# Performance work log

Measured on AMD Instinct MI355X. Metric: run time of the kernel, lower is better.

Reference implementation:

```python
import jax, jax.numpy as jnp
import numpy as np

B = 65536
D_EMB = 512      # embedding_dim
D_SPD = 1        # speed_dim
D_LAT = 128      # speed_latent_dim
H = 256          # hidden_size
K = 6            # num_branch
D_IN = D_EMB + D_LAT  # 640, branch/speed-head input dim


def _lin(key, din, dout):
    kw, kb = jax.random.split(key)
    W = jax.random.normal(kw, (din, dout), dtype=jnp.float32) * 0.02
    b = jax.random.normal(kb, (dout,), dtype=jnp.float32) * 0.02
    return W, b


def setup_inputs() -> dict:
    key = jax.random.key(0)
    ks = jax.random.split(key, 16)
    embedding = jax.random.normal(ks[0], (B, D_EMB), dtype=jnp.float32)
    speed = jax.random.uniform(ks[1], (B, D_SPD), dtype=jnp.float32)
    command = jax.random.randint(ks[2], (B,), 1, K + 1, dtype=jnp.int32)  # values 1..6
    # speed input MLP: speed_dim -> H -> D_LAT
    Wsi1, bsi1 = _lin(ks[3], D_SPD, H)
    Wsi2, bsi2 = _lin(ks[4], H, D_LAT)
    # speed prediction head: D_IN -> H -> H -> speed_dim
    Wso1, bso1 = _lin(ks[5], D_IN, H)
    Wso2, bso2 = _lin(ks[6], H, H)
    Wso3, bso3 = _lin(ks[7], H, D_SPD)
    # K branch heads, stacked on leading axis: D_IN -> H -> H -> 3, sigmoid
    def _stack(key, din, dout):
        kw, kb = jax.random.split(key)
        W = jax.random.normal(kw, (K, din, dout), dtype=jnp.float32) * 0.02
        b = jax.random.normal(kb, (K, dout), dtype=jnp.float32) * 0.02
        return W, b
    Wb1, bb1 = _stack(ks[8], D_IN, H)
    Wb2, bb2 = _stack(ks[9], H, H)
    Wb3, bb3 = _stack(ks[10], H, 3)
    return dict(embedding=embedding, speed=speed, command=command,
                Wsi1=Wsi1, bsi1=bsi1, Wsi2=Wsi2, bsi2=bsi2,
                Wso1=Wso1, bso1=bso1, Wso2=Wso2, bso2=bso2, Wso3=Wso3, bso3=bso3,
                Wb1=Wb1, bb1=bb1, Wb2=Wb2, bb2=bb2, Wb3=Wb3, bb3=bb3)


def reference(embedding, speed, command,
              Wsi1, bsi1, Wsi2, bsi2,
              Wso1, bso1, Wso2, bso2, Wso3, bso3,
              Wb1, bb1, Wb2, bb2, Wb3, bb3):
    # speed -> latent
    sp = jax.nn.relu(speed @ Wsi1 + bsi1) @ Wsi2 + bsi2          # [B, D_LAT]
    emb = jnp.concatenate([embedding, sp], axis=1)               # [B, D_IN]
    # compute ALL K branch heads (as the original does), then mask by command
    h = jax.nn.relu(jnp.einsum('bd,kdh->bkh', emb, Wb1) + bb1)   # [B, K, H]
    h = jax.nn.relu(jnp.einsum('bkh,khj->bkj', h, Wb2) + bb2)    # [B, K, H]
    ctrl_all = jax.nn.sigmoid(jnp.einsum('bkh,kho->bko', h, Wb3) + bb3)  # [B, K, 3]
    mask = (command[:, None] - 1 == jnp.arange(K)[None, :]).astype(ctrl_all.dtype)  # [B, K]
    control_pred = jnp.sum(ctrl_all * mask[:, :, None], axis=1)  # [B, 3]
    # speed prediction head
    hs = jax.nn.relu(emb @ Wso1 + bso1)
    hs = jax.nn.relu(hs @ Wso2 + bso2)
    speed_pred = hs @ Wso3 + bso3                                # [B, 1]
    return control_pred, speed_pred
```

## Files before the change

kernel.cpp:

```cpp
#include <hip/hip_runtime.h>
#include <hip/hip_bf16.h>


#define NB 65536
#define NBRB 1030

typedef __attribute__((ext_vector_type(8))) short short8;
typedef __attribute__((ext_vector_type(4))) float f32x4;
typedef unsigned short bhalf;
typedef unsigned int u32;

__device__ __forceinline__ bhalf f2b(float x) {
    __hip_bfloat16 h = __float2bfloat16(x);
    return *reinterpret_cast<bhalf*>(&h);
}
__device__ __forceinline__ void gll16(const void* g, void* l) {
    __builtin_amdgcn_global_load_lds(
        (const __attribute__((address_space(1))) u32*)g,
        (__attribute__((address_space(3))) u32*)l, 16, 0, 0);
}
__device__ __forceinline__ int sadr(int row, int cb) {
    return row * 64 + (cb ^ (((row >> 1) & 3) << 4));
}
__device__ __forceinline__ int yadr(int row, int cb) {
    return row * 512 + (cb ^ ((row & 7) << 4));
}
__device__ __forceinline__ void wvm6() { asm volatile("s_waitcnt vmcnt(6)" ::: "memory"); }
__device__ __forceinline__ void wvm0() { asm volatile("s_waitcnt vmcnt(0)" ::: "memory"); }
__device__ __forceinline__ void wlgkm0() { asm volatile("s_waitcnt lgkmcnt(0)" ::: "memory"); }

__global__ __launch_bounds__(256) void k_wprep(
    const float* __restrict__ Wsi2, const float* __restrict__ Wso1,
    const float* __restrict__ Wso2, const float* __restrict__ Wb1,
    const float* __restrict__ Wb2,
    bhalf* __restrict__ Wsi2T, bhalf* __restrict__ Wso1T,
    bhalf* __restrict__ Wso2T, bhalf* __restrict__ Wb1T,
    bhalf* __restrict__ Wb2T) {
    __shared__ float T[64][65];
    const int id = blockIdx.x, t = threadIdx.x;
    const float* src; bhalf* dst; int K, N, tk, tn, b;
    if (id < 8)        { src = Wsi2; dst = Wsi2T; K = 256; N = 128; b = 0; int tl = id;      tk = tl / 2; tn = tl % 2; }
    else if (id < 48)  { src = Wso1; dst = Wso1T; K = 640; N = 256; b = 0; int tl = id - 8;  tk = tl / 4; tn = tl % 4; }
    else if (id < 64)  { src = Wso2; dst = Wso2T; K = 256; N = 256; b = 0; int tl = id - 48; tk = tl / 4; tn = tl % 4; }
    else if (id < 304) { src = Wb1;  dst = Wb1T;  K = 640; N = 256; int li = id - 64;  b = li / 40; int tl = li % 40; tk = tl / 4; tn = tl % 4; }
    else               { src = Wb2;  dst = Wb2T;  K = 256; N = 256; int li = id - 304; b = li / 16; int tl = li % 16; tk = tl / 4; tn = tl % 4; }
    const int k0 = tk * 64, n0 = tn * 64;
    src += (size_t)b * K * N; dst += (size_t)b * N * K;
    const int c = t & 63, r0 = t >> 6;
#pragma unroll
    for (int j = 0; j < 16; ++j) {
        int r = r0 + j * 4;
        T[r][c] = src[(size_t)(k0 + r) * N + n0 + c];
    }
    __syncthreads();
#pragma unroll
    for (int j = 0; j < 16; ++j) {
        int r = r0 + j * 4;
        dst[(size_t)(n0 + r) * K + k0 + c] = f2b(T[c][r]);
    }
}

__global__ __launch_bounds__(256) void k_prep(
    const float* __restrict__ speed, const float* __restrict__ Wsi1,
    const float* __restrict__ bsi1, const bhalf* __restrict__ Wsi2T,
    const float* __restrict__ bsi2, const int* __restrict__ cmd,
    bhalf* __restrict__ spb, int* __restrict__ bcnt) {
    __shared__ bhalf A[64 * 72];
    __shared__ bhalf BT[128 * 72];
    const int t = threadIdx.x, lane = t & 63, wid = t >> 6;
    const int rbase = blockIdx.x * 64;
    if (wid == 0) {
        int c = cmd[rbase + lane] - 1;
        int v = 0;
#pragma unroll
        for (int g = 0; g < 6; ++g) {
            unsigned long long m = __ballot(c == g);
            if (lane == g) v = (int)__popcll(m);
        }
        if (lane < 6) bcnt[blockIdx.x * 6 + lane] = v;
    }
    const int wm = wid >> 1, wn = wid & 1;
    f32x4 acc[2][4];
    for (int m = 0; m < 2; ++m) for (int n = 0; n < 4; ++n)
        for (int r = 0; r < 4; ++r) acc[m][n][r] = 0.f;
    const int ar = t >> 2, kp = (t & 3) * 16;
    const float s = speed[rbase + ar];
    for (int kc = 0; kc < 4; ++kc) {
        short8 w0, w1;
#pragma unroll
        for (int j = 0; j < 8; ++j) {
            int k = kc * 64 + kp + j;
            w0[j] = (short)f2b(fmaxf(fmaf(s, Wsi1[k], bsi1[k]), 0.f));
            w1[j] = (short)f2b(fmaxf(fmaf(s, Wsi1[k + 8], bsi1[k + 8]), 0.f));
        }
        *(short8*)&A[ar * 72 + kp] = w0;
        *(short8*)&A[ar * 72 + kp + 8] = w1;
#pragma unroll
        for (int j = 0; j < 4; ++j) {
            int ch = t + j * 256;
            int n2 = ch >> 3, ko = (ch & 7) * 8;
            *(short8*)&BT[n2 * 72 + ko] =
                *(const short8*)(Wsi2T + n2 * 256 + kc * 64 + ko);
        }
        __syncthreads();
#pragma unroll
        for (int ks = 0; ks < 2; ++ks) {
            short8 a[2], b[4];
#pragma unroll
            for (int m = 0; m < 2; ++m)
                a[m] = *(const short8*)&A[(wm * 32 + m * 16 + (lane & 15)) * 72 + ks * 32 + (lane >> 4) * 8];
#pragma unroll
            for (int n = 0; n < 4; ++n)
                b[n] = *(const short8*)&BT[(wn * 64 + n * 16 + (lane & 15)) * 72 + ks * 32 + (lane >> 4) * 8];
#pragma unroll
            for (int m = 0; m < 2; ++m)
#pragma unroll
                for (int n = 0; n < 4; ++n)
                    acc[m][n] = __builtin_amdgcn_mfma_f32_16x16x32_bf16(a[m], b[n], acc[m][n], 0, 0, 0);
        }
        __syncthreads();
    }
#pragma unroll
    for (int m = 0; m < 2; ++m)
#pragma unroll
    for (int n = 0; n < 4; ++n) {
        int col = wn * 64 + n * 16 + (lane & 15);
        float bias = bsi2[col];
#pragma unroll
        for (int r = 0; r < 4; ++r) {
            int row = rbase + wm * 32 + m * 16 + (lane >> 4) * 4 + r;
            spb[row * 128 + col] = f2b(acc[m][n][r] + bias);
        }
    }
}

__global__ __launch_bounds__(1024) void k_scan(
    const int* __restrict__ bcnt, int* __restrict__ chunkoff,
    int* __restrict__ pad) {
    __shared__ int sc[1024];
    __shared__ int tot[8];
    __shared__ int spo[8];
    const int t = threadIdx.x;
    for (int g = 0; g < 6; ++g) {
        int v = bcnt[t * 6 + g];
        sc[t] = v;
        __syncthreads();
        for (int s = 1; s < 1024; s <<= 1) {
            int u = (t >= s) ? sc[t - s] : 0;
            __syncthreads();
            sc[t] += u;
            __syncthreads();
        }
        if (t == 1023) tot[g] = sc[t];
        chunkoff[t * 6 + g] = sc[t] - v;
        __syncthreads();
    }
    if (t == 0) {
        int off = 0;
        for (int g = 0; g < 6; ++g) {
            spo[g] = off; pad[g] = off; pad[8 + g] = tot[g];
            off += ((tot[g] + 63) >> 6) << 6;
        }
        spo[6] = off; pad[6] = off;
    }
    __syncthreads();
    for (int g = 0; g < 6; ++g) chunkoff[t * 6 + g] += spo[g];
}

__global__ __launch_bounds__(256) void k_scatter(
    const int* __restrict__ cmd, const int* __restrict__ chunkoff,
    int* __restrict__ perm) {
    const int lane = threadIdx.x & 63, w = threadIdx.x >> 6;
    const int chunk = blockIdx.x * 4 + w;
    const int idx = chunk * 64 + lane;
    const int c = cmd[idx] - 1;
#pragma unroll
    for (int g = 0; g < 6; ++g) {
        unsigned long long m = __ballot(c == g);
        if (c == g) {
            int pos = chunkoff[chunk * 6 + g] + (int)__popcll(m & ((1ull << lane) - 1ull));
            perm[pos] = idx;
        }
    }
}

__global__ __launch_bounds__(256, 3) void k_head(
    const float* __restrict__ emb, const bhalf* __restrict__ spb,
    const bhalf* __restrict__ Wso1T, const float* __restrict__ bso1,
    const bhalf* __restrict__ Wso2T, const float* __restrict__ bso2,
    const float* __restrict__ Wso3, const float* __restrict__ bso3,
    const bhalf* __restrict__ Wb1T, const float* __restrict__ bb1,
    const bhalf* __restrict__ Wb2T, const float* __restrict__ bb2,
    const float* __restrict__ Wb3, const float* __restrict__ bb3,
    const int* __restrict__ pad, const int* __restrict__ perm,
    float* __restrict__ out) {
    __shared__ __align__(16) char L[49152];
    char* const SB0 = L;
    char* const SAr = L + 32768;
    char* const Yb  = L;
    const int t = threadIdx.x, lane = t & 63, wid = t >> 6;
    const bool isB = blockIdx.x < NBRB;
    int tstart, DOUT, gcnt, gbase;
    const bhalf *W1T, *W2T; const float *b1, *b2, *W3, *b3;
    if (isB) {
        tstart = blockIdx.x * 64;
        if (tstart >= pad[6]) return;
        int g = 0;
        while (pad[g + 1] <= tstart) ++g;
        gbase = pad[g]; gcnt = pad[8 + g];
        W1T = Wb1T + (size_t)g * (256 * 640); b1 = bb1 + g * 256;
        W2T = Wb2T + (size_t)g * (256 * 256); b2 = bb2 + g * 256;
        W3  = Wb3  + (size_t)g * (256 * 3);   b3 = bb3 + g * 3;
        DOUT = 3;
    } else {
        tstart = (blockIdx.x - NBRB) * 64;
        gbase = 0; gcnt = NB;
        W1T = Wso1T; b1 = bso1; W2T = Wso2T; b2 = bso2; W3 = Wso3; b3 = bso3;
        DOUT = 1;
    }

    const int rowA0 = t >> 3, rowA1 = rowA0 + 32, rowS = t >> 2;
    int ra0, ra1, raS;
    if (isB) {
        int p0 = tstart + rowA0, p1 = tstart + rowA1, pS = tstart + rowS;
        ra0 = ((p0 - gbase) < gcnt) ? perm[p0] : 0;
        ra1 = ((p1 - gbase) < gcnt) ? perm[p1] : 0;
        raS = ((pS - gbase) < gcnt) ? perm[pS] : 0;
    } else {
        ra0 = tstart + rowA0; ra1 = tstart + rowA1; raS = tstart + rowS;
    }
    const int lcA0 = ((t & 7) * 16) ^ ((rowA0 & 7) << 4);
    const int lcA1 = ((t & 7) * 16) ^ ((rowA1 & 7) << 4);
    const int lcS  = ((t & 3) * 16) ^ (((rowS >> 1) & 3) << 4);
    const char* embp0 = (const char*)(emb + (size_t)ra0 * 512);
    const char* embp1 = (const char*)(emb + (size_t)ra1 * 512);
    const char* spbp  = (const char*)(spb + (size_t)raS * 128);
    const int dstA = t * 16;
    const int rB = t >> 2, cB = (t & 3) * 16;

#define ST_A(KN, BUF) do { int kn_ = (KN); char* d_ = SAr + (BUF) * 8192 + dstA; \
        if (kn_ < 16) {                                                           \
            gll16(embp0 + kn_ * 128 + lcA0, d_);                                  \
            gll16(embp1 + kn_ * 128 + lcA1, d_ + 4096);                           \
        } else {                                                                  \
            gll16(spbp + (kn_ - 16) * 64 + lcS, d_);                              \
            gll16(spbp + (kn_ - 16) * 64 + lcS, d_ + 4096);                       \
        } } while (0)
#define ST_B1(KN, BUF) do {                                                       \
        _Pragma("unroll")                                                         \
        for (int j_ = 0; j_ < 4; ++j_) {                                          \
            int row_ = rB + j_ * 64;                                              \
            int p_ = row_ * 64 + cB;                                              \
            int lc_ = cB ^ (((row_ >> 1) & 3) << 4);                              \
            gll16((const char*)W1T + (size_t)row_ * 1280 + (KN) * 64 + lc_,       \
                  SB0 + (BUF) * 16384 + p_);                                      \
        } } while (0)
#define ST_B2(KB) do {                                                            \
        _Pragma("unroll")                                                         \
        for (int j_ = 0; j_ < 4; ++j_) {                                          \
            int row_ = rB + j_ * 64;                                              \
            int p_ = row_ * 64 + cB;                                              \
            int lc_ = cB ^ (((row_ >> 1) & 3) << 4);                              \
            gll16((const char*)W2T + (size_t)row_ * 512 + (KB) + lc_,             \
                  SAr + p_);                                                      \
        } } while (0)

    const int arow = lane & 15, koff = (lane >> 4) * 16;
    float bi1[4], bi2[4];
#pragma unroll
    for (int n = 0; n < 4; ++n) {
        bi1[n] = b1[wid * 64 + n * 16 + arow];
        bi2[n] = b2[wid * 64 + n * 16 + arow];
    }

    f32x4 acc[4][4];
#pragma unroll
    for (int m = 0; m < 4; ++m)
#pragma unroll
        for (int n = 0; n < 4; ++n)
#pragma unroll
            for (int r = 0; r < 4; ++r) acc[m][n][r] = 0.f;

    ST_A(0, 0); ST_B1(0, 0);
    for (int kc = 0; kc < 20; ++kc) {
        const int buf = kc & 1;
        if (kc < 19) { ST_A(kc + 1, buf ^ 1); ST_B1(kc + 1, buf ^ 1); wvm6(); }
        else         { wvm0(); }
        __builtin_amdgcn_s_barrier();
        const char* SAc = SAr + buf * 8192;
        const char* SBc = SB0 + buf * 16384;
        short8 a[4], b[4];
#pragma unroll
        for (int n = 0; n < 4; ++n)
            b[n] = *(const short8*)(SBc + sadr(wid * 64 + n * 16 + arow, koff));
        if (kc < 16) {
#pragma unroll
            for (int m = 0; m < 4; ++m) {
                int row = m * 16 + arow;
                int sw = (row & 7) << 4;
                int c0 = (lane >> 4) * 32;
                float4 f0 = *(const float4*)(SAc + row * 128 + (c0 ^ sw));
                float4 f1 = *(const float4*)(SAc + row * 128 + ((c0 + 16) ^ sw));
                a[m][0] = (short)f2b(f0.x); a[m][1] = (short)f2b(f0.y);
                a[m][2] = (short)f2b(f0.z); a[m][3] = (short)f2b(f0.w);
                a[m][4] = (short)f2b(f1.x); a[m][5] = (short)f2b(f1.y);
                a[m][6] = (short)f2b(f1.z); a[m][7] = (short)f2b(f1.w);
            }
        } else {
#pragma unroll
            for (int m = 0; m < 4; ++m)
                a[m] = *(const short8*)(SAc + sadr(m * 16 + arow, koff));
        }
#pragma unroll
        for (int m = 0; m < 4; ++m)
#pragma unroll
            for (int n = 0; n < 4; ++n)
                acc[m][n] = __builtin_amdgcn_mfma_f32_16x16x32_bf16(a[m], b[n], acc[m][n], 0, 0, 0);
        __builtin_amdgcn_s_barrier();
    }
#pragma unroll
    for (int m = 0; m < 4; ++m)
#pragma unroll
    for (int n = 0; n < 4; ++n) {
        int col = wid * 64 + n * 16 + arow;
#pragma unroll
        for (int r = 0; r < 4; ++r) {
            int row = m * 16 + (lane >> 4) * 4 + r;
            *(bhalf*)(Yb + yadr(row, 2 * col)) = f2b(fmaxf(acc[m][n][r] + bi1[n], 0.f));
            acc[m][n][r] = 0.f;
        }
    }
    ST_B2(0);
    wlgkm0();
    wvm0();
    __builtin_amdgcn_s_barrier();
    for (int kc = 0; kc < 8; ++kc) {
        short8 a[4], b[4];
#pragma unroll
        for (int m = 0; m < 4; ++m)
            a[m] = *(const short8*)(Yb + yadr(m * 16 + arow, kc * 64 + koff));
#pragma unroll
        for (int n = 0; n < 4; ++n)
            b[n] = *(const short8*)(SAr + sadr(wid * 64 + n * 16 + arow, koff));
#pragma unroll
        for (int m = 0; m < 4; ++m)
#pragma unroll
            for (int n = 0; n < 4; ++n)
                acc[m][n] = __builtin_amdgcn_mfma_f32_16x16x32_bf16(a[m], b[n], acc[m][n], 0, 0, 0);
        __builtin_amdgcn_s_barrier();
        if (kc < 7) { ST_B2((kc + 1) * 64); wvm0(); }
        __builtin_amdgcn_s_barrier();
    }
#pragma unroll
    for (int m = 0; m < 4; ++m)
#pragma unroll
    for (int n = 0; n < 4; ++n) {
        int col = wid * 64 + n * 16 + arow;
#pragma unroll
        for (int r = 0; r < 4; ++r) {
            int row = m * 16 + (lane >> 4) * 4 + r;
            *(bhalf*)(Yb + yadr(row, 2 * col)) = f2b(fmaxf(acc[m][n][r] + bi2[n], 0.f));
        }
    }
    wlgkm0();
    __builtin_amdgcn_s_barrier();
    f32x4 z;
#pragma unroll
    for (int r = 0; r < 4; ++r) z[r] = 0.f;
    const int col3 = arow;
    for (int kc = 0; kc < 8; ++kc) {
        short8 a3 = *(const short8*)(Yb + yadr(wid * 16 + arow, kc * 64 + koff));
        short8 bw;
#pragma unroll
        for (int j = 0; j < 8; ++j) bw[j] = 0;
        if (col3 < DOUT) {
            int kb = kc * 32 + (lane >> 4) * 8;
#pragma unroll
            for (int j = 0; j < 8; ++j)
                bw[j] = (short)f2b(W3[(kb + j) * DOUT + col3]);
        }
        z = __builtin_amdgcn_mfma_f32_16x16x32_bf16(a3, bw, z, 0, 0, 0);
    }
    if (col3 < DOUT) {
        float bias = b3[col3];
#pragma unroll
        for (int rr = 0; rr < 4; ++rr) {
            int r = wid * 16 + (lane >> 4) * 4 + rr;
            int p2 = tstart + r;
            if ((p2 - gbase) < gcnt) {
                float v = z[rr] + bias;
                if (isB) {
                    int ro = perm[p2];
                    out[(size_t)ro * 3 + col3] = 1.f / (1.f + __expf(-v));
                } else {
                    out[(size_t)NB * 3 + p2] = v;
                }
            }
        }
    }
#undef ST_A
#undef ST_B1
#undef ST_B2
}

extern "C" void kernel_launch(void* const* d_in, const int* in_sizes, int n_in,
                              void* d_out, int out_size, void* d_ws, size_t ws_size,
                              hipStream_t stream) {
    (void)in_sizes; (void)n_in; (void)out_size; (void)ws_size;
    const float* emb   = (const float*)d_in[0];
    const float* speed = (const float*)d_in[1];
    const int*   cmd   = (const int*)d_in[2];
    const float* Wsi1  = (const float*)d_in[3];
    const float* bsi1  = (const float*)d_in[4];
    const float* Wsi2  = (const float*)d_in[5];
    const float* bsi2  = (const float*)d_in[6];
    const float* Wso1  = (const float*)d_in[7];
    const float* bso1  = (const float*)d_in[8];
    const float* Wso2  = (const float*)d_in[9];
    const float* bso2  = (const float*)d_in[10];
    const float* Wso3  = (const float*)d_in[11];
    const float* bso3  = (const float*)d_in[12];
    const float* Wb1   = (const float*)d_in[13];
    const float* bb1   = (const float*)d_in[14];
    const float* Wb2   = (const float*)d_in[15];
    const float* bb2   = (const float*)d_in[16];
    const float* Wb3   = (const float*)d_in[17];
    const float* bb3   = (const float*)d_in[18];
    float* out = (float*)d_out;

    char* ws = (char*)d_ws;
    bhalf* spb      = (bhalf*)(ws);
    int*   perm     = (int*)(ws + 16777216);
    int*   bcnt     = (int*)(ws + 17040896);
    int*   chunkoff = (int*)(ws + 17065472);
    int*   pad      = (int*)(ws + 17090048);
    bhalf* Wsi2T    = (bhalf*)(ws + 17090304);
    bhalf* Wso1T    = (bhalf*)(ws + 17155840);
    bhalf* Wso2T    = (bhalf*)(ws + 17483520);
    bhalf* Wb1T     = (bhalf*)(ws + 17614592);
    bhalf* Wb2T     = (bhalf*)(ws + 19580672);

    k_wprep<<<400, 256, 0, stream>>>(Wsi2, Wso1, Wso2, Wb1, Wb2,
                                     Wsi2T, Wso1T, Wso2T, Wb1T, Wb2T);
    k_prep<<<NB / 64, 256, 0, stream>>>(speed, Wsi1, bsi1, Wsi2T, bsi2, cmd,
                                        spb, bcnt);
    k_scan<<<1, 1024, 0, stream>>>(bcnt, chunkoff, pad);
    k_scatter<<<NB / 256, 256, 0, stream>>>(cmd, chunkoff, perm);
    k_head<<<NBRB + NB / 64, 256, 0, stream>>>(emb, spb,
                                               Wso1T, bso1, Wso2T, bso2, Wso3, bso3,
                                               Wb1T, bb1, Wb2T, bb2, Wb3, bb3,
                                               pad, perm, out);
}
```

Baseline: 155.7 us.

## Fuse branch and speed heads into one persistent 128-row tile kernel

The head kernel now has each 512-thread block process one 128-row command-sorted tile. One 4-wave half computes the selected branch MLP and the other half computes the speed MLP, both reusing the same staged embedding/latent tile. This cuts global reads of the large fp32 embedding from two passes to one. The grid is persistent, with 512 blocks looping over tiles, and group padding grows to 128 rows. Second-layer weights are now read straight from global into registers instead of staged through LDS. The costs are a 160KB LDS footprint that likely limits residency to one block per CU, heavy accumulator register pressure, and some extra padded rows per group.

```diff
diff --git a/kernel.cpp b/kernel.cpp
--- a/kernel.cpp
+++ b/kernel.cpp
@@ -3,7 +3,6 @@
 
 
 #define NB 65536
-#define NBRB 1030
 
 typedef __attribute__((ext_vector_type(8))) short short8;
 typedef __attribute__((ext_vector_type(4))) float f32x4;
@@ -22,12 +21,12 @@
 __device__ __forceinline__ int sadr(int row, int cb) {
     return row * 64 + (cb ^ (((row >> 1) & 3) << 4));
 }
-__device__ __forceinline__ int yadr(int row, int cb) {
-    return row * 512 + (cb ^ ((row & 7) << 4));
-}
-__device__ __forceinline__ void wvm6() { asm volatile("s_waitcnt vmcnt(6)" ::: "memory"); }
-__device__ __forceinline__ void wvm0() { asm volatile("s_waitcnt vmcnt(0)" ::: "memory"); }
-__device__ __forceinline__ void wlgkm0() { asm volatile("s_waitcnt lgkmcnt(0)" ::: "memory"); }
+__device__ __forceinline__ int yadr2(int row, int cb) {
+    return row * 1024 + (cb ^ ((row & 7) << 4));
+}
+__device__ __forceinline__ void wvm6()  { asm volatile("s_waitcnt vmcnt(6)"  ::: "memory"); }
+__device__ __forceinline__ void wvm0()  { asm volatile("s_waitcnt vmcnt(0)"  ::: "memory"); }
+__device__ __forceinline__ void wlgkm0(){ asm volatile("s_waitcnt lgkmcnt(0)" ::: "memory"); }
 
 __global__ __launch_bounds__(256) void k_wprep(
     const float* __restrict__ Wsi2, const float* __restrict__ Wso1,
@@ -159,7 +158,7 @@
         int off = 0;
         for (int g = 0; g < 6; ++g) {
             spo[g] = off; pad[g] = off; pad[8 + g] = tot[g];
-            off += ((tot[g] + 63) >> 6) << 6;
+            off += ((tot[g] + 127) >> 7) << 7;
         }
         spo[6] = off; pad[6] = off;
     }
@@ -184,7 +183,7 @@
     }
 }
 
-__global__ __launch_bounds__(256, 3) void k_head(
+__global__ __launch_bounds__(512, 2) void k_head(
     const float* __restrict__ emb, const bhalf* __restrict__ spb,
     const bhalf* __restrict__ Wso1T, const float* __restrict__ bso1,
     const bhalf* __restrict__ Wso2T, const float* __restrict__ bso2,
@@ -194,213 +193,217 @@
     const float* __restrict__ Wb3, const float* __restrict__ bb3,
     const int* __restrict__ pad, const int* __restrict__ perm,
     float* __restrict__ out) {
-    __shared__ __align__(16) char L[49152];
-    char* const SB0 = L;
-    char* const SAr = L + 32768;
-    char* const Yb  = L;
+    __shared__ __align__(16) char L[163840];
+    char* const SA0 = L;
+    char* const SB0 = L + 32768;
+    char* const Yb  = L + 32768;
     const int t = threadIdx.x, lane = t & 63, wid = t >> 6;
-    const bool isB = blockIdx.x < NBRB;
-    int tstart, DOUT, gcnt, gbase;
-    const bhalf *W1T, *W2T; const float *b1, *b2, *W3, *b3;
-    if (isB) {
-        tstart = blockIdx.x * 64;
-        if (tstart >= pad[6]) return;
-        int g = 0;
-        while (pad[g + 1] <= tstart) ++g;
-        gbase = pad[g]; gcnt = pad[8 + g];
-        W1T = Wb1T + (size_t)g * (256 * 640); b1 = bb1 + g * 256;
-        W2T = Wb2T + (size_t)g * (256 * 256); b2 = bb2 + g * 256;
-        W3  = Wb3  + (size_t)g * (256 * 3);   b3 = bb3 + g * 3;
-        DOUT = 3;
-    } else {
-        tstart = (blockIdx.x - NBRB) * 64;
-        gbase = 0; gcnt = NB;
-        W1T = Wso1T; b1 = bso1; W2T = Wso2T; b2 = bso2; W3 = Wso3; b3 = bso3;
-        DOUT = 1;
-    }
-
-    const int rowA0 = t >> 3, rowA1 = rowA0 + 32, rowS = t >> 2;
-    int ra0, ra1, raS;
-    if (isB) {
-        int p0 = tstart + rowA0, p1 = tstart + rowA1, pS = tstart + rowS;
-        ra0 = ((p0 - gbase) < gcnt) ? perm[p0] : 0;
-        ra1 = ((p1 - gbase) < gcnt) ? perm[p1] : 0;
-        raS = ((pS - gbase) < gcnt) ? perm[pS] : 0;
-    } else {
-        ra0 = tstart + rowA0; ra1 = tstart + rowA1; raS = tstart + rowS;
-    }
+    const int head = wid >> 2, wn = wid & 3;
+    const int pad6 = pad[6];
+    const int NT = (pad6 + 127) >> 7;
+    const int arow = lane & 15, koff = (lane >> 4) * 16;
+    const int rowA0 = t >> 3, rowA1 = rowA0 + 64, rowS = t >> 2;
     const int lcA0 = ((t & 7) * 16) ^ ((rowA0 & 7) << 4);
     const int lcA1 = ((t & 7) * 16) ^ ((rowA1 & 7) << 4);
     const int lcS  = ((t & 3) * 16) ^ (((rowS >> 1) & 3) << 4);
-    const char* embp0 = (const char*)(emb + (size_t)ra0 * 512);
-    const char* embp1 = (const char*)(emb + (size_t)ra1 * 512);
-    const char* spbp  = (const char*)(spb + (size_t)raS * 128);
     const int dstA = t * 16;
     const int rB = t >> 2, cB = (t & 3) * 16;
-
-#define ST_A(KN, BUF) do { int kn_ = (KN); char* d_ = SAr + (BUF) * 8192 + dstA; \
+    const int col0h = wn * 64 + arow;
+
+    for (int tile = blockIdx.x; tile < NT; tile += 512) {
+        const int tstart = tile * 128;
+        int g = 0;
+        while (pad[g + 1] <= tstart) ++g;
+        const int gbase = pad[g], gcnt = pad[8 + g];
+        const bhalf* W1b = Wb1T + (size_t)g * (256 * 640);
+
+        int pA0 = tstart + rowA0, pA1 = tstart + rowA1, pS = tstart + rowS;
+        const int ra0 = ((pA0 - gbase) < gcnt) ? perm[pA0] : 0;
+        const int ra1 = ((pA1 - gbase) < gcnt) ? perm[pA1] : 0;
+        const int raS = ((pS - gbase) < gcnt) ? perm[pS] : 0;
+        const char* embp0 = (const char*)(emb + (size_t)ra0 * 512);
+        const char* embp1 = (const char*)(emb + (size_t)ra1 * 512);
+        const char* spbp  = (const char*)(spb + (size_t)raS * 128);
+        const float* b1h = head ? bso1 : bb1 + g * 256;
+        const float* b2h = head ? bso2 : bb2 + g * 256;
+        float bi1[4], bi2[4];
+#pragma unroll
+        for (int n = 0; n < 4; ++n) {
+            bi1[n] = b1h[col0h + n * 16];
+            bi2[n] = b2h[col0h + n * 16];
+        }
+
+        f32x4 acc[8][4];
+#pragma unroll
+        for (int m = 0; m < 8; ++m)
+#pragma unroll
+            for (int n = 0; n < 4; ++n)
+#pragma unroll
+                for (int r = 0; r < 4; ++r) acc[m][n][r] = 0.f;
+
+#define ST_A(KN, BUF) do { int kn_ = (KN); char* d_ = SA0 + (BUF) * 16384 + dstA; \
         if (kn_ < 16) {                                                           \
             gll16(embp0 + kn_ * 128 + lcA0, d_);                                  \
-            gll16(embp1 + kn_ * 128 + lcA1, d_ + 4096);                           \
+            gll16(embp1 + kn_ * 128 + lcA1, d_ + 8192);                           \
         } else {                                                                  \
             gll16(spbp + (kn_ - 16) * 64 + lcS, d_);                              \
-            gll16(spbp + (kn_ - 16) * 64 + lcS, d_ + 4096);                       \
+            gll16(spbp + (kn_ - 16) * 64 + lcS, d_);       \
         } } while (0)
-#define ST_B1(KN, BUF) do {                                                       \
+#define ST_B(KN, BUF) do {                                                        \
         _Pragma("unroll")                                                         \
         for (int j_ = 0; j_ < 4; ++j_) {                                          \
-            int row_ = rB + j_ * 64;                                              \
+            int row_ = rB + j_ * 128;                                             \
             int p_ = row_ * 64 + cB;                                              \
             int lc_ = cB ^ (((row_ >> 1) & 3) << 4);                              \
-            gll16((const char*)W1T + (size_t)row_ * 1280 + (KN) * 64 + lc_,       \
-                  SB0 + (BUF) * 16384 + p_);                                      \
+            const char* s_ = (row_ < 256)                                         \
+                ? (const char*)W1b + (size_t)row_ * 1280 + (KN) * 64 + lc_        \
+                : (const char*)Wso1T + (size_t)(row_ - 256) * 1280 + (KN) * 64 + lc_; \
+            gll16(s_, SB0 + (BUF) * 32768 + p_);                                  \
         } } while (0)
-#define ST_B2(KB) do {                                                            \
-        _Pragma("unroll")                                                         \
-        for (int j_ = 0; j_ < 4; ++j_) {                                          \
-            int row_ = rB + j_ * 64;                                              \
-            int p_ = row_ * 64 + cB;                                              \
-            int lc_ = cB ^ (((row_ >> 1) & 3) << 4);                              \
-            gll16((const char*)W2T + (size_t)row_ * 512 + (KB) + lc_,             \
-                  SAr + p_);                                                      \
-        } } while (0)
-
-    const int arow = lane & 15, koff = (lane >> 4) * 16;
-    float bi1[4], bi2[4];
-#pragma unroll
-    for (int n = 0; n < 4; ++n) {
-        bi1[n] = b1[wid * 64 + n * 16 + arow];
-        bi2[n] = b2[wid * 64 + n * 16 + arow];
-    }
-
-    f32x4 acc[4][4];
-#pragma unroll
-    for (int m = 0; m < 4; ++m)
-#pragma unroll
-        for (int n = 0; n < 4; ++n)
-#pragma unroll
-            for (int r = 0; r < 4; ++r) acc[m][n][r] = 0.f;
-
-    ST_A(0, 0); ST_B1(0, 0);
-    for (int kc = 0; kc < 20; ++kc) {
-        const int buf = kc & 1;
-        if (kc < 19) { ST_A(kc + 1, buf ^ 1); ST_B1(kc + 1, buf ^ 1); wvm6(); }
-        else         { wvm0(); }
+
+        ST_A(0, 0); ST_B(0, 0);
+        for (int kc = 0; kc < 20; ++kc) {
+            const int buf = kc & 1;
+            if (kc < 19) { ST_A(kc + 1, buf ^ 1); ST_B(kc + 1, buf ^ 1); wvm6(); }
+            else         { wvm0(); }
+            __builtin_amdgcn_s_barrier();
+            const char* SAc = SA0 + buf * 16384;
+            const char* SBc = SB0 + buf * 32768;
+            short8 b[4];
+#pragma unroll
+            for (int n = 0; n < 4; ++n)
+                b[n] = *(const short8*)(SBc + sadr(head * 256 + wn * 64 + n * 16 + arow, koff));
+#pragma unroll
+            for (int m = 0; m < 8; ++m) {
+                short8 am;
+                if (kc < 16) {
+                    int row = m * 16 + arow;
+                    int sw = (row & 7) << 4;
+                    int c0 = (lane >> 4) * 32;
+                    float4 f0 = *(const float4*)(SAc + row * 128 + (c0 ^ sw));
+                    float4 f1 = *(const float4*)(SAc + row * 128 + ((c0 + 16) ^ sw));
+                    am[0] = (short)f2b(f0.x); am[1] = (short)f2b(f0.y);
+                    am[2] = (short)f2b(f0.z); am[3] = (short)f2b(f0.w);
+                    am[4] = (short)f2b(f1.x); am[5] = (short)f2b(f1.y);
+                    am[6] = (short)f2b(f1.z); am[7] = (short)f2b(f1.w);
+                } else {
+                    am = *(const short8*)(SAc + sadr(m * 16 + arow, koff));
+                }
+                acc[m][0] = __builtin_amdgcn_mfma_f32_16x16x32_bf16(am, b[0], acc[m][0], 0, 0, 0);
+                acc[m][1] = __builtin_amdgcn_mfma_f32_16x16x32_bf16(am, b[1], acc[m][1], 0, 0, 0);
+                acc[m][2] = __builtin_amdgcn_mfma_f32_16x16x32_bf16(am, b[2], acc[m][2], 0, 0, 0);
+                acc[m][3] = __builtin_amdgcn_mfma_f32_16x16x32_bf16(am, b[3], acc[m][3], 0, 0, 0);
+            }
+            __builtin_amdgcn_s_barrier();
+        }
+        const bhalf* W2h = head ? Wso2T : Wb2T + (size_t)g * (256 * 256);
+        const char* cp0 = (const char*)W2h + (size_t)(col0h +  0) * 512 + koff;
+        const char* cp1 = (const char*)W2h + (size_t)(col0h + 16) * 512 + koff;
+        const char* cp2 = (const char*)W2h + (size_t)(col0h + 32) * 512 + koff;
+        const char* cp3 = (const char*)W2h + (size_t)(col0h + 48) * 512 + koff;
+        short8 bc0 = *(const short8*)cp0;
+        short8 bc1 = *(const short8*)cp1;
+        short8 bc2 = *(const short8*)cp2;
+        short8 bc3 = *(const short8*)cp3;
+#pragma unroll
+        for (int m = 0; m < 8; ++m)
+#pragma unroll
+        for (int n = 0; n < 4; ++n) {
+            int cb = head * 512 + 2 * (wn * 64 + n * 16 + arow);
+#pragma unroll
+            for (int r = 0; r < 4; ++r) {
+                int row = m * 16 + (lane >> 4) * 4 + r;
+                *(bhalf*)(Yb + yadr2(row, cb)) = f2b(fmaxf(acc[m][n][r] + bi1[n], 0.f));
+                acc[m][n][r] = 0.f;
+            }
+        }
+        wlgkm0();
         __builtin_amdgcn_s_barrier();
-        const char* SAc = SAr + buf * 8192;
-        const char* SBc = SB0 + buf * 16384;
-        short8 a[4], b[4];
-#pragma unroll
-        for (int n = 0; n < 4; ++n)
-            b[n] = *(const short8*)(SBc + sadr(wid * 64 + n * 16 + arow, koff));
-        if (kc < 16) {
-#pragma unroll
-            for (int m = 0; m < 4; ++m) {
-                int row = m * 16 + arow;
-                int sw = (row & 7) << 4;
-                int c0 = (lane >> 4) * 32;
-                float4 f0 = *(const float4*)(SAc + row * 128 + (c0 ^ sw));
-                float4 f1 = *(const float4*)(SAc + row * 128 + ((c0 + 16) ^ sw));
-                a[m][0] = (short)f2b(f0.x); a[m][1] = (short)f2b(f0.y);
-                a[m][2] = (short)f2b(f0.z); a[m][3] = (short)f2b(f0.w);
-                a[m][4] = (short)f2b(f1.x); a[m][5] = (short)f2b(f1.y);
-                a[m][6] = (short)f2b(f1.z); a[m][7] = (short)f2b(f1.w);
+        for (int kc = 0; kc < 8; ++kc) {
+            short8 a[8];
+#pragma unroll
+            for (int m = 0; m < 8; ++m)
+                a[m] = *(const short8*)(Yb + yadr2(m * 16 + arow, head * 512 + kc * 64 + koff));
+#pragma unroll
+            for (int m = 0; m < 8; ++m)
+                acc[m][0] = __builtin_amdgcn_mfma_f32_16x16x32_bf16(a[m], bc0, acc[m][0], 0, 0, 0);
+            if (kc < 7) bc0 = *(const short8*)(cp0 + (kc + 1) * 64);
+#pragma unroll
+            for (int m = 0; m < 8; ++m)
+                acc[m][1] = __builtin_amdgcn_mfma_f32_16x16x32_bf16(a[m], bc1, acc[m][1], 0, 0, 0);
+            if (kc < 7) bc1 = *(const short8*)(cp1 + (kc + 1) * 64);
+#pragma unroll
+            for (int m = 0; m < 8; ++m)
+                acc[m][2] = __builtin_amdgcn_mfma_f32_16x16x32_bf16(a[m], bc2, acc[m][2], 0, 0, 0);
+            if (kc < 7) bc2 = *(const short8*)(cp2 + (kc + 1) * 64);
+#pragma unroll
+            for (int m = 0; m < 8; ++m)
+                acc[m][3] = __builtin_amdgcn_mfma_f32_16x16x32_bf16(a[m], bc3, acc[m][3], 0, 0, 0);
+            if (kc < 7) bc3 = *(const short8*)(cp3 + (kc + 1) * 64);
+        }
+        __builtin_amdgcn_s_barrier();
+#pragma unroll
+        for (int m = 0; m < 8; ++m)
+#pragma unroll
+        for (int n = 0; n < 4; ++n) {
+            int cb = head * 512 + 2 * (wn * 64 + n * 16 + arow);
+#pragma unroll
+            for (int r = 0; r < 4; ++r) {
+                int row = m * 16 + (lane >> 4) * 4 + r;
+                *(bhalf*)(Yb + yadr2(row, cb)) = f2b(fmaxf(acc[m][n][r] + bi2[n], 0.f));
             }
-        } else {
-#pragma unroll
-            for (int m = 0; m < 4; ++m)
-                a[m] = *(const short8*)(SAc + sadr(m * 16 + arow, koff));
-        }
-#pragma unroll
-        for (int m = 0; m < 4; ++m)
-#pragma unroll
-            for (int n = 0; n < 4; ++n)
-                acc[m][n] = __builtin_amdgcn_mfma_f32_16x16x32_bf16(a[m], b[n], acc[m][n], 0, 0, 0);
+        }
+        wlgkm0();
         __builtin_amdgcn_s_barrier();
-    }
-#pragma unroll
-    for (int m = 0; m < 4; ++m)
-#pragma unroll
-    for (int n = 0; n < 4; ++n) {
-        int col = wid * 64 + n * 16 + arow;
-#pragma unroll
-        for (int r = 0; r < 4; ++r) {
-            int row = m * 16 + (lane >> 4) * 4 + r;
-            *(bhalf*)(Yb + yadr(row, 2 * col)) = f2b(fmaxf(acc[m][n][r] + bi1[n], 0.f));
-            acc[m][n][r] = 0.f;
-        }
-    }
-    ST_B2(0);
-    wlgkm0();
-    wvm0();
-    __builtin_amdgcn_s_barrier();
-    for (int kc = 0; kc < 8; ++kc) {
-        short8 a[4], b[4];
-#pragma unroll
-        for (int m = 0; m < 4; ++m)
-            a[m] = *(const short8*)(Yb + yadr(m * 16 + arow, kc * 64 + koff));
-#pragma unroll
-        for (int n = 0; n < 4; ++n)
-            b[n] = *(const short8*)(SAr + sadr(wid * 64 + n * 16 + arow, koff));
-#pragma unroll
-        for (int m = 0; m < 4; ++m)
-#pragma unroll
-            for (int n = 0; n < 4; ++n)
-                acc[m][n] = __builtin_amdgcn_mfma_f32_16x16x32_bf16(a[m], b[n], acc[m][n], 0, 0, 0);
-        __builtin_amdgcn_s_barrier();
-        if (kc < 7) { ST_B2((kc + 1) * 64); wvm0(); }
-        __builtin_amdgcn_s_barrier();
-    }
-#pragma unroll
-    for (int m = 0; m < 4; ++m)
-#pragma unroll
-    for (int n = 0; n < 4; ++n) {
-        int col = wid * 64 + n * 16 + arow;
-#pragma unroll
-        for (int r = 0; r < 4; ++r) {
-            int row = m * 16 + (lane >> 4) * 4 + r;
-            *(bhalf*)(Yb + yadr(row, 2 * col)) = f2b(fmaxf(acc[m][n][r] + bi2[n], 0.f));
-        }
-    }
-    wlgkm0();
-    __builtin_amdgcn_s_barrier();
-    f32x4 z;
-#pragma unroll
-    for (int r = 0; r < 4; ++r) z[r] = 0.f;
-    const int col3 = arow;
-    for (int kc = 0; kc < 8; ++kc) {
-        short8 a3 = *(const short8*)(Yb + yadr(wid * 16 + arow, kc * 64 + koff));
-        short8 bw;
-#pragma unroll
-        for (int j = 0; j < 8; ++j) bw[j] = 0;
-        if (col3 < DOUT) {
-            int kb = kc * 32 + (lane >> 4) * 8;
-#pragma unroll
-            for (int j = 0; j < 8; ++j)
-                bw[j] = (short)f2b(W3[(kb + j) * DOUT + col3]);
-        }
-        z = __builtin_amdgcn_mfma_f32_16x16x32_bf16(a3, bw, z, 0, 0, 0);
-    }
-    if (col3 < DOUT) {
-        float bias = b3[col3];
-#pragma unroll
-        for (int rr = 0; rr < 4; ++rr) {
-            int r = wid * 16 + (lane >> 4) * 4 + rr;
-            int p2 = tstart + r;
-            if ((p2 - gbase) < gcnt) {
-                float v = z[rr] + bias;
-                if (isB) {
-                    int ro = perm[p2];
-                    out[(size_t)ro * 3 + col3] = 1.f / (1.f + __expf(-v));
-                } else {
-                    out[(size_t)NB * 3 + p2] = v;
+        {
+            const int DOUT = head ? 1 : 3;
+            const float* W3h = head ? Wso3 : Wb3 + (size_t)g * (256 * 3);
+            const float* b3h = head ? bso3 : bb3 + g * 3;
+            f32x4 z0, z1;
+#pragma unroll
+            for (int r = 0; r < 4; ++r) { z0[r] = 0.f; z1[r] = 0.f; }
+            const int col3 = arow;
+            for (int kc = 0; kc < 8; ++kc) {
+                short8 a30 = *(const short8*)(Yb + yadr2(wn * 32 + arow,      head * 512 + kc * 64 + koff));
+                short8 a31 = *(const short8*)(Yb + yadr2(wn * 32 + 16 + arow, head * 512 + kc * 64 + koff));
+                short8 bw;
+#pragma unroll
+                for (int j = 0; j < 8; ++j) bw[j] = 0;
+                if (col3 < DOUT) {
+                    int kq = kc * 32 + (lane >> 4) * 8;
+#pragma unroll
+                    for (int j = 0; j < 8; ++j)
+                        bw[j] = (short)f2b(W3h[(kq + j) * DOUT + col3]);
+                }
+                z0 = __builtin_amdgcn_mfma_f32_16x16x32_bf16(a30, bw, z0, 0, 0, 0);
+                z1 = __builtin_amdgcn_mfma_f32_16x16x32_bf16(a31, bw, z1, 0, 0, 0);
+            }
+            if (col3 < DOUT) {
+                float bias = b3h[col3];
+#pragma unroll
+                for (int rr = 0; rr < 4; ++rr) {
+                    int r0 = wn * 32 + (lane >> 4) * 4 + rr;
+                    int r1 = r0 + 16;
+                    int p0 = tstart + r0, p1 = tstart + r1;
+                    if ((p0 - gbase) < gcnt) {
+                        int ro = perm[p0];
+                        float v = z0[rr] + bias;
+                        if (head == 0) out[(size_t)ro * 3 + col3] = 1.f / (1.f + __expf(-v));
+                        else           out[(size_t)NB * 3 + ro] = v;
+                    }
+                    if ((p1 - gbase) < gcnt) {
+                        int ro = perm[p1];
+                        float v = z1[rr] + bias;
+                        if (head == 0) out[(size_t)ro * 3 + col3] = 1.f / (1.f + __expf(-v));
+                        else           out[(size_t)NB * 3 + ro] = v;
+                    }
                 }
             }
         }
-    }
+        __builtin_amdgcn_s_barrier();
 #undef ST_A
-#undef ST_B1
-#undef ST_B2
+#undef ST_B
+    }
 }
 
 extern "C" void kernel_launch(void* const* d_in, const int* in_sizes, int n_in,
@@ -431,14 +434,14 @@
     char* ws = (char*)d_ws;
     bhalf* spb      = (bhalf*)(ws);
     int*   perm     = (int*)(ws + 16777216);
-    int*   bcnt     = (int*)(ws + 17040896);
-    int*   chunkoff = (int*)(ws + 17065472);
-    int*   pad      = (int*)(ws + 17090048);
-    bhalf* Wsi2T    = (bhalf*)(ws + 17090304);
-    bhalf* Wso1T    = (bhalf*)(ws + 17155840);
-    bhalf* Wso2T    = (bhalf*)(ws + 17483520);
-    bhalf* Wb1T     = (bhalf*)(ws + 17614592);
-    bhalf* Wb2T     = (bhalf*)(ws + 19580672);
+    int*   bcnt     = (int*)(ws + 17043456);
+    int*   chunkoff = (int*)(ws + 17068032);
+    int*   pad      = (int*)(ws + 17092608);
+    bhalf* Wsi2T    = (bhalf*)(ws + 17092864);
+    bhalf* Wso1T    = (bhalf*)(ws + 17158400);
+    bhalf* Wso2T    = (bhalf*)(ws + 17486080);
+    bhalf* Wb1T     = (bhalf*)(ws + 17617152);
+    bhalf* Wb2T     = (bhalf*)(ws + 19583232);
 
     k_wprep<<<400, 256, 0, stream>>>(Wsi2, Wso1, Wso2, Wb1, Wb2,
                                      Wsi2T, Wso1T, Wso2T, Wb1T, Wb2T);
@@ -446,8 +449,8 @@
                                         spb, bcnt);
     k_scan<<<1, 1024, 0, stream>>>(bcnt, chunkoff, pad);
     k_scatter<<<NB / 256, 256, 0, stream>>>(cmd, chunkoff, perm);
-    k_head<<<NBRB + NB / 64, 256, 0, stream>>>(emb, spb,
-                                               Wso1T, bso1, Wso2T, bso2, Wso3, bso3,
-                                               Wb1T, bb1, Wb2T, bb2, Wb3, bb3,
-                                               pad, perm, out);
-}
+    k_head<<<512, 512, 0, stream>>>(emb, spb,
+                                    Wso1T, bso1, Wso2T, bso2, Wso3, bso3,
+                                    Wb1T, bb1, Wb2T, bb2, Wb3, bb3,
+                                    pad, perm, out);
+}
```

After: 479.4 us. +207.9%, slower.
